# Kernel tuning notes

Measured on AMD Instinct MI355X. Metric: run time of the kernel, lower is better.

Reference implementation:

```python
import jax, jax.numpy as jnp
import numpy as np

N_NODES = 50000
N_EDGES = 800000
D_IN = 256
D_HID = 256
N_CLASSES = 32
N_GRAPHS = 64


def _sage_conv(x, src, dst, W_l, b_l, W_r, num_nodes):
    # PyG SAGEConv (mean aggr, root_weight=True):
    # out = lin_l(mean_{j->i} x_j) + lin_r(x_i)
    msg = x[src]                                                   # [E, d]
    agg = jax.ops.segment_sum(msg, dst, num_segments=num_nodes)   # [N, d]
    cnt = jax.ops.segment_sum(jnp.ones((src.shape[0], 1), x.dtype), dst,
                              num_segments=num_nodes)             # [N, 1]
    agg = agg / jnp.maximum(cnt, 1.0)
    return agg @ W_l + b_l + x @ W_r


def setup_inputs() -> dict:
    key = jax.random.key(0)
    ks = jax.random.split(key, 12)
    x = jax.random.normal(ks[0], (N_NODES, D_IN), dtype=jnp.float32)
    edge_index = jax.random.randint(ks[1], (2, N_EDGES), 0, N_NODES, dtype=jnp.int64)
    batch = jnp.sort(jax.random.randint(ks[2], (N_NODES,), 0, N_GRAPHS, dtype=jnp.int64))
    s1 = 1.0 / np.sqrt(D_IN)
    s2 = 1.0 / np.sqrt(D_HID)
    return {
        "x": x,
        "edge_index": edge_index,
        "batch": batch,
        "W1_l": jax.random.uniform(ks[3], (D_IN, D_HID), jnp.float32, -s1, s1),
        "b1": jax.random.uniform(ks[4], (D_HID,), jnp.float32, -s1, s1),
        "W1_r": jax.random.uniform(ks[5], (D_IN, D_HID), jnp.float32, -s1, s1),
        "W2_l": jax.random.uniform(ks[6], (D_HID, D_HID), jnp.float32, -s2, s2),
        "b2": jax.random.uniform(ks[7], (D_HID,), jnp.float32, -s2, s2),
        "W2_r": jax.random.uniform(ks[8], (D_HID, D_HID), jnp.float32, -s2, s2),
        "Wc": jax.random.uniform(ks[9], (D_HID, N_CLASSES), jnp.float32, -s2, s2),
        "bc": jax.random.uniform(ks[10], (N_CLASSES,), jnp.float32, -s2, s2),
    }


def reference(x, edge_index, batch, W1_l, b1, W1_r, W2_l, b2, W2_r, Wc, bc):
    src, dst = edge_index[0], edge_index[1]
    h = jax.nn.relu(_sage_conv(x, src, dst, W1_l, b1, W1_r, N_NODES))
    h = jax.nn.relu(_sage_conv(h, src, dst, W2_l, b2, W2_r, N_NODES))
    # global mean pool over graphs
    gsum = jax.ops.segment_sum(h, batch, num_segments=N_GRAPHS)        # [G, d]
    gcnt = jax.ops.segment_sum(jnp.ones((h.shape[0], 1), h.dtype), batch,
                               num_segments=N_GRAPHS)                  # [G, 1]
    g = gsum / jnp.maximum(gcnt, 1.0)
    return g @ Wc + bc
```

## Files before the change

kernel.cpp:

```cpp
#include <hip/hip_runtime.h>
#include <stdint.h>

#define NNODES 50000
#define NEDGES 800000
#define DDIM 256
#define NCLS 32
#define NGRAPH 64
#define NSCANB ((NNODES + 255) / 256)
#define HISTB ((NEDGES + 255) / 256)
#define HISTB8 (HISTB * 8)
#define CVTXB ((NNODES * 64 + 255) / 256)
#define CVTWB (2 * 256 * 512 / 256)
#define NPXCD (NNODES / 8)

typedef short bf16x8 __attribute__((ext_vector_type(8)));
typedef float f32x4 __attribute__((ext_vector_type(4)));
typedef unsigned short u16x4 __attribute__((ext_vector_type(4)));
typedef unsigned short u16x8 __attribute__((ext_vector_type(8)));

typedef __attribute__((address_space(1))) const char glb_c;
typedef __attribute__((address_space(3))) char lds_c;


__device__ __forceinline__ unsigned short f2b(float f) {
  uint32_t u = __builtin_bit_cast(uint32_t, f);
  u += 0x7FFFu + ((u >> 16) & 1u);
  return (unsigned short)(u >> 16);
}
__device__ __forceinline__ float b2f(unsigned short u) {
  return __builtin_bit_cast(float, (uint32_t)u << 16);
}
__device__ __forceinline__ float blo(uint32_t u) {
  return __builtin_bit_cast(float, u << 16);
}
__device__ __forceinline__ float bhi(uint32_t u) {
  return __builtin_bit_cast(float, u & 0xFFFF0000u);
}

__device__ __forceinline__ void gload16(const void* g, const void* l) {
  __builtin_amdgcn_global_load_lds((glb_c*)g, (lds_c*)l, 16, 0, 0);
}


__global__ void k_setup(const int* __restrict__ dst, int* __restrict__ cnt,
                        const float* __restrict__ x, unsigned short* __restrict__ xb,
                        const float* __restrict__ W1l, const float* __restrict__ W1r,
                        const float* __restrict__ W2l, const float* __restrict__ W2r,
                        unsigned short* __restrict__ WT1, unsigned short* __restrict__ WT2) {
  int b = blockIdx.x;
  if (b < HISTB8) {
    int xcd = b & 7;
    int e = (b >> 3) * 256 + threadIdx.x;
    if (e < NEDGES) {
      int d = dst[e];
      if ((unsigned)(d - xcd * NPXCD) < (unsigned)NPXCD) atomicAdd(&cnt[d], 1);
    }
  } else if (b < HISTB8 + CVTXB) {
    int i = (b - HISTB8) * 256 + threadIdx.x;
    if (i < NNODES * 64) {
      int seg = i & 7;
      int rr = i >> 3;
      int slab = rr / NNODES;
      int r = rr - slab * NNODES;
      float4 v = *(const float4*)(x + (size_t)r * DDIM + slab * 32 + seg * 4);
      u16x4 o;
      o.x = f2b(v.x); o.y = f2b(v.y); o.z = f2b(v.z); o.w = f2b(v.w);
      *(u16x4*)(xb + (size_t)i * 4) = o;
    }
  } else {
    int idx = (b - HISTB8 - CVTXB) * 256 + threadIdx.x;
    int which = idx >> 17;
    int id2 = idx & 131071;
    int n = id2 >> 9, k = id2 & 511;
    const float* Wl = which ? W2l : W1l;
    const float* Wr = which ? W2r : W1r;
    unsigned short* WT = which ? WT2 : WT1;
    float v = (k < 256) ? Wl[k * 256 + n] : Wr[(k - 256) * 256 + n];
    WT[id2] = f2b(v);
  }
}


__global__ void k_scan1(const int* __restrict__ cnt, int* __restrict__ bsum) {
  int b = blockIdx.x;
  int i = b * 256 + threadIdx.x;
  int lane = threadIdx.x & 63, wid = threadIdx.x >> 6;
  int v = (i < NNODES) ? cnt[i] : 0;
#pragma unroll
  for (int o = 1; o < 64; o <<= 1) v += __shfl_xor(v, o, 64);
  __shared__ int ws[4];
  if (lane == 0) ws[wid] = v;
  __syncthreads();
  if (threadIdx.x == 0) bsum[b] = ws[0] + ws[1] + ws[2] + ws[3];
}

__global__ void k_scan2(const int* __restrict__ bsum, int* __restrict__ boffs) {
  int tid = threadIdx.x, lane = tid & 63, wid = tid >> 6;
  int v = (tid < NSCANB) ? bsum[tid] : 0;
  int s = v;
#pragma unroll
  for (int o = 1; o < 64; o <<= 1) {
    int t = __shfl_up(s, o, 64);
    if (lane >= o) s += t;
  }
  __shared__ int ws[4];
  if (lane == 63) ws[wid] = s;
  __syncthreads();
  int add = 0;
  for (int w = 0; w < wid; ++w) add += ws[w];
  if (tid < NSCANB) boffs[tid] = s + add - v;
}

__global__ void k_scan3(const int* __restrict__ cnt, const int* __restrict__ boffs,
                        int* __restrict__ rowptr, int* __restrict__ cursor,
                        float* __restrict__ gsum, const int* __restrict__ batch,
                        int* __restrict__ gcnt) {
  int b = blockIdx.x;
  if (b < NSCANB) {
    int i = b * 256 + threadIdx.x;
    int lane = threadIdx.x & 63, wid = threadIdx.x >> 6;
    int v = (i < NNODES) ? cnt[i] : 0;
    int s = v;
#pragma unroll
    for (int o = 1; o < 64; o <<= 1) {
      int t = __shfl_up(s, o, 64);
      if (lane >= o) s += t;
    }
    __shared__ int ws[4];
    if (lane == 63) ws[wid] = s;
    __syncthreads();
    int add = boffs[b];
    for (int w = 0; w < wid; ++w) add += ws[w];
    int incl = s + add;
    if (i < NNODES) {
      rowptr[i + 1] = incl;
      cursor[i] = incl - v;
    }
    if (b == 0 && threadIdx.x == 0) rowptr[0] = 0;
  } else if (b == NSCANB) {
    for (int i = threadIdx.x; i < NGRAPH * DDIM; i += 256) gsum[i] = 0.f;
  } else {
    int g = threadIdx.x;
    if (g < NGRAPH) {
      int lo = 0, hi = NNODES;
      while (lo < hi) { int m = (lo + hi) >> 1; if (batch[m] < g) lo = m + 1; else hi = m; }
      int lo2 = lo, hi2 = NNODES;
      while (lo2 < hi2) { int m = (lo2 + hi2) >> 1; if (batch[m] < g + 1) lo2 = m + 1; else hi2 = m; }
      gcnt[g] = lo2 - lo;
    }
  }
}

__global__ void k_fill(const int* __restrict__ src, const int* __restrict__ dst,
                       int* __restrict__ cursor, int* __restrict__ col) {
  int b = blockIdx.x;
  int xcd = b & 7;
  int e = (b >> 3) * 256 + threadIdx.x;
  if (e < NEDGES) {
    int d = dst[e];
    if ((unsigned)(d - xcd * NPXCD) < (unsigned)NPXCD) {
      int p = atomicAdd(&cursor[d], 1);
      col[p] = src[e];
    }
  }
}


__global__ void k_agg(const unsigned short* __restrict__ feat,
                      const int* __restrict__ rowptr, const int* __restrict__ col,
                      unsigned short* __restrict__ out) {
  int g = blockIdx.x & 7;
  int nb = blockIdx.x >> 3;
  int wv = threadIdx.x >> 6, lane = threadIdx.x & 63;
  int ns = lane >> 2;
  int seg = lane & 3;
  int node = nb * 64 + wv * 16 + ns;
  bool valid = node < NNODES;
  int nn = valid ? node : NNODES - 1;
  int s = rowptr[nn], e = rowptr[nn + 1];
  if (!valid) e = s;
  const unsigned short* slabp = feat + (size_t)g * NNODES * 32 + seg * 8;
  float a[8] = {0.f}, b[8] = {0.f};
  int last = e - 1;
  for (int i = s; i < e; i += 8) {
    uint4 vv[8];
#pragma unroll
    for (int j = 0; j < 8; ++j) {
      int idx = i + j;
      int cidx = (idx <= last) ? idx : last;
      int ce = col[cidx];
      uint4 r = *(const uint4*)(slabp + (size_t)ce * 32);
      if (idx > last) { r.x = 0u; r.y = 0u; r.z = 0u; r.w = 0u; }
      vv[j] = r;
    }
#pragma unroll
    for (int j = 0; j < 8; j += 2) {
      a[0] += blo(vv[j].x); a[1] += bhi(vv[j].x);
      a[2] += blo(vv[j].y); a[3] += bhi(vv[j].y);
      a[4] += blo(vv[j].z); a[5] += bhi(vv[j].z);
      a[6] += blo(vv[j].w); a[7] += bhi(vv[j].w);
      b[0] += blo(vv[j + 1].x); b[1] += bhi(vv[j + 1].x);
      b[2] += blo(vv[j + 1].y); b[3] += bhi(vv[j + 1].y);
      b[4] += blo(vv[j + 1].z); b[5] += bhi(vv[j + 1].z);
      b[6] += blo(vv[j + 1].w); b[7] += bhi(vv[j + 1].w);
    }
  }
  if (valid) {
    float inv = (e > s) ? 1.f / (float)(e - s) : 0.f;
    u16x8 o;
#pragma unroll
    for (int j = 0; j < 8; ++j) o[j] = f2b((a[j] + b[j]) * inv);
    unsigned short* op = out + ((size_t)g * NNODES + node) * 32 + seg * 8;
    __builtin_nontemporal_store(o, (u16x8*)op);
  }
}


__global__ void k_gemm(const unsigned short* __restrict__ Aagg,
                       const unsigned short* __restrict__ Aroot,
                       const unsigned short* __restrict__ WT,
                       const float* __restrict__ bias,
                       unsigned short* __restrict__ out) {
  __shared__ unsigned short As[128 * 32];
  __shared__ unsigned short Bs[128 * 32];
  int m0 = blockIdx.x * 128;
  int n0 = blockIdx.y * 128;
  int tid = threadIdx.x, lane = tid & 63, wv = tid >> 6;
  int wm = wv >> 1, wn = wv & 1;

  f32x4 acc[4][4];
#pragma unroll
  for (int m = 0; m < 4; ++m)
#pragma unroll
    for (int n = 0; n < 4; ++n) acc[m][n] = (f32x4)0.f;

  for (int kt = 0; kt < 16; ++kt) {
    int k = kt * 32;
    const unsigned short* Abase = (k < 256) ? Aagg : Aroot;
    int slab = (k & 255) >> 5;
    const unsigned short* Aslab = Abase + (size_t)slab * NNODES * 32;
#pragma unroll
    for (int q = 0; q < 2; ++q) {
      int idx = q * 256 + tid;
      int row = idx >> 2, seg = idx & 3;
      int gr = m0 + row;
      if (gr >= NNODES) gr = NNODES - 1;
      const unsigned short* sp = Aslab + (size_t)gr * 32 + seg * 8;
      gload16(sp, (const char*)As + (q * 256 + wv * 64) * 16);
    }
#pragma unroll
    for (int q = 0; q < 2; ++q) {
      int idx = q * 256 + tid;
      int row = idx >> 2, seg = idx & 3;
      const unsigned short* sp = WT + (size_t)(n0 + row) * 512 + k + seg * 8;
      gload16(sp, (const char*)Bs + (q * 256 + wv * 64) * 16);
    }
    __syncthreads();

    bf16x8 af[4], bfr[4];
    int kb = (lane >> 4) * 8;
    int rA = wm * 64 + (lane & 15);
    int rB = wn * 64 + (lane & 15);
#pragma unroll
    for (int m = 0; m < 4; ++m) af[m] = *(const bf16x8*)&As[(rA + m * 16) * 32 + kb];
#pragma unroll
    for (int n = 0; n < 4; ++n) bfr[n] = *(const bf16x8*)&Bs[(rB + n * 16) * 32 + kb];
#pragma unroll
    for (int m = 0; m < 4; ++m)
#pragma unroll
      for (int n = 0; n < 4; ++n)
        acc[m][n] = __builtin_amdgcn_mfma_f32_16x16x32_bf16(af[m], bfr[n], acc[m][n], 0, 0, 0);
    __syncthreads();
  }

  int rbase = m0 + wm * 64 + (lane >> 4) * 4;
  int cbase = n0 + wn * 64 + (lane & 15);
#pragma unroll
  for (int n = 0; n < 4; ++n) {
    int cc = cbase + n * 16;
    float bv = bias[cc];
    size_t sbase = (size_t)(cc >> 5) * NNODES * 32 + (cc & 31);
#pragma unroll
    for (int m = 0; m < 4; ++m) {
#pragma unroll
      for (int j = 0; j < 4; ++j) {
        int r = rbase + m * 16 + j;
        if (r < NNODES) {
          float v = acc[m][n][j] + bv;
          v = fmaxf(v, 0.f);
          out[sbase + (size_t)r * 32] = f2b(v);
        }
      }
    }
  }
}


#define GSUM_WAVES 1024
__global__ void k_gsum(const unsigned short* __restrict__ h2,
                       const int* __restrict__ batch,
                       float* __restrict__ gsum) {
  int wave = (blockIdx.x * blockDim.x + threadIdx.x) >> 6;
  int lane = threadIdx.x & 63;
  const int per = (NNODES + GSUM_WAVES - 1) / GSUM_WAVES;
  int r0 = wave * per;
  int r1 = r0 + per; if (r1 > NNODES) r1 = NNODES;
  if (r0 >= r1) return;
  int slab = lane >> 3, seg = lane & 7;
  int cb = slab * 32 + seg * 4;
  const unsigned short* sp = h2 + (size_t)slab * NNODES * 32 + seg * 4;
  float a0 = 0.f, a1 = 0.f, a2 = 0.f, a3 = 0.f;
  int cur = batch[r0];
  for (int r = r0; r < r1; ++r) {
    int g = batch[r];
    if (g != cur) {
      float* gp = gsum + cur * DDIM + cb;
      atomicAdd(gp + 0, a0); atomicAdd(gp + 1, a1);
      atomicAdd(gp + 2, a2); atomicAdd(gp + 3, a3);
      a0 = a1 = a2 = a3 = 0.f;
      cur = g;
    }
    u16x4 v = *(const u16x4*)(sp + (size_t)r * 32);
    a0 += b2f(v.x); a1 += b2f(v.y); a2 += b2f(v.z); a3 += b2f(v.w);
  }
  float* gp = gsum + cur * DDIM + cb;
  atomicAdd(gp + 0, a0); atomicAdd(gp + 1, a1);
  atomicAdd(gp + 2, a2); atomicAdd(gp + 3, a3);
}

__global__ void k_cls(const float* __restrict__ gsum, const int* __restrict__ cnt,
                      const float* __restrict__ Wc, const float* __restrict__ bc,
                      float* __restrict__ out) {
  int g = blockIdx.x;
  __shared__ float colmean[DDIM];
  int c = threadIdx.x;
  int n = cnt[g];
  float inv = (n > 0) ? 1.f / (float)n : 0.f;
  colmean[c] = gsum[g * DDIM + c] * inv;
  __syncthreads();
  if (c < NCLS) {
    float o = bc[c];
#pragma unroll 4
    for (int k = 0; k < DDIM; ++k) o += colmean[k] * Wc[k * NCLS + c];
    out[g * NCLS + c] = o;
  }
}


extern "C" void kernel_launch(void* const* d_in, const int* in_sizes, int n_in,
                              void* d_out, int out_size, void* d_ws, size_t ws_size,
                              hipStream_t stream) {
  const float* x    = (const float*)d_in[0];
  const int* eidx   = (const int*)d_in[1];
  const int* batch  = (const int*)d_in[2];
  const float* W1l  = (const float*)d_in[3];
  const float* b1   = (const float*)d_in[4];
  const float* W1r  = (const float*)d_in[5];
  const float* W2l  = (const float*)d_in[6];
  const float* b2   = (const float*)d_in[7];
  const float* W2r  = (const float*)d_in[8];
  const float* Wc   = (const float*)d_in[9];
  const float* bc   = (const float*)d_in[10];
  float* out = (float*)d_out;

  const int* esrc = eidx;
  const int* edst = eidx + NEDGES;

  char* w = (char*)d_ws;
  size_t off = 0;
  auto alloc = [&](size_t bytes) -> char* {
    char* p = w + off;
    off = (off + bytes + 255) & ~(size_t)255;
    return p;
  };
  int* rowptr = (int*)alloc((NNODES + 1) * sizeof(int));
  int* cursor = (int*)alloc(NNODES * sizeof(int));
  int* col    = (int*)alloc(NEDGES * sizeof(int));
  unsigned short* xb   = (unsigned short*)alloc((size_t)NNODES * DDIM * 2);
  unsigned short* h1b  = (unsigned short*)alloc((size_t)NNODES * DDIM * 2);
  unsigned short* aggb = (unsigned short*)alloc((size_t)NNODES * DDIM * 2);
  unsigned short* WT1  = (unsigned short*)alloc(512 * 256 * 2);
  unsigned short* WT2  = (unsigned short*)alloc(512 * 256 * 2);
  float* gsum = (float*)alloc(NGRAPH * DDIM * sizeof(float));
  int* gcnt   = (int*)alloc(NGRAPH * sizeof(int));
  int* bsum   = (int*)alloc(NSCANB * sizeof(int));
  int* boffs  = (int*)alloc(NSCANB * sizeof(int));

  hipMemsetAsync(cursor, 0, NNODES * sizeof(int), stream);
  k_setup<<<HISTB8 + CVTXB + CVTWB, 256, 0, stream>>>(edst, cursor, x, xb,
                                                      W1l, W1r, W2l, W2r, WT1, WT2);
  k_scan1<<<NSCANB, 256, 0, stream>>>(cursor, bsum);
  k_scan2<<<1, 256, 0, stream>>>(bsum, boffs);
  k_scan3<<<NSCANB + 2, 256, 0, stream>>>(cursor, boffs, rowptr, cursor,
                                          gsum, batch, gcnt);
  k_fill<<<HISTB8, 256, 0, stream>>>(esrc, edst, cursor, col);

  dim3 ggrid((NNODES + 127) / 128, 2);
  int agg_grid = ((NNODES + 63) / 64) * 8;

  k_agg<<<agg_grid, 256, 0, stream>>>(xb, rowptr, col, aggb);
  k_gemm<<<ggrid, 256, 0, stream>>>(aggb, xb, WT1, b1, h1b);

  k_agg<<<agg_grid, 256, 0, stream>>>(h1b, rowptr, col, aggb);
  k_gemm<<<ggrid, 256, 0, stream>>>(aggb, h1b, WT2, b2, xb);

  k_gsum<<<GSUM_WAVES / 4, 256, 0, stream>>>(xb, batch, gsum);
  k_cls<<<NGRAPH, 256, 0, stream>>>(gsum, gcnt, Wc, bc, out);
}
```

Measured before the change: 293.5 us.

## Widen GEMM tile to full N with 512 threads; move conversion into fill kernel

The GEMM now uses 512-thread blocks, each covering 128 rows and all 256 output columns. A-tiles are loaded once per row block instead of once per column half, at the cost of a larger B tile in LDS. The x and weight bf16 conversion moves from the histogram kernel into the CSR fill kernel, and the x conversion now reads rows coalesced and scatters into slab layout. The histogram gets its own kernel and count buffer. The aim is to cut redundant A reads and balance the setup kernels.

```diff
diff --git a/kernel.cpp b/kernel.cpp
--- a/kernel.cpp
+++ b/kernel.cpp
@@ -9,7 +9,7 @@
 #define NSCANB ((NNODES + 255) / 256)
 #define HISTB ((NEDGES + 255) / 256)
 #define HISTB8 (HISTB * 8)
-#define CVTXB ((NNODES * 64 + 255) / 256)
+#define CVTXB (NNODES * 64 / 256)
 #define CVTWB (2 * 256 * 512 / 256)
 #define NPXCD (NNODES / 8)
 
@@ -42,44 +42,15 @@
 }
 
 
-__global__ void k_setup(const int* __restrict__ dst, int* __restrict__ cnt,
-                        const float* __restrict__ x, unsigned short* __restrict__ xb,
-                        const float* __restrict__ W1l, const float* __restrict__ W1r,
-                        const float* __restrict__ W2l, const float* __restrict__ W2r,
-                        unsigned short* __restrict__ WT1, unsigned short* __restrict__ WT2) {
+__global__ void k_hist(const int* __restrict__ dst, int* __restrict__ cnt) {
   int b = blockIdx.x;
-  if (b < HISTB8) {
-    int xcd = b & 7;
-    int e = (b >> 3) * 256 + threadIdx.x;
-    if (e < NEDGES) {
-      int d = dst[e];
-      if ((unsigned)(d - xcd * NPXCD) < (unsigned)NPXCD) atomicAdd(&cnt[d], 1);
-    }
-  } else if (b < HISTB8 + CVTXB) {
-    int i = (b - HISTB8) * 256 + threadIdx.x;
-    if (i < NNODES * 64) {
-      int seg = i & 7;
-      int rr = i >> 3;
-      int slab = rr / NNODES;
-      int r = rr - slab * NNODES;
-      float4 v = *(const float4*)(x + (size_t)r * DDIM + slab * 32 + seg * 4);
-      u16x4 o;
-      o.x = f2b(v.x); o.y = f2b(v.y); o.z = f2b(v.z); o.w = f2b(v.w);
-      *(u16x4*)(xb + (size_t)i * 4) = o;
-    }
-  } else {
-    int idx = (b - HISTB8 - CVTXB) * 256 + threadIdx.x;
-    int which = idx >> 17;
-    int id2 = idx & 131071;
-    int n = id2 >> 9, k = id2 & 511;
-    const float* Wl = which ? W2l : W1l;
-    const float* Wr = which ? W2r : W1r;
-    unsigned short* WT = which ? WT2 : WT1;
-    float v = (k < 256) ? Wl[k * 256 + n] : Wr[(k - 256) * 256 + n];
-    WT[id2] = f2b(v);
-  }
-}
-
+  int xcd = b & 7;
+  int e = (b >> 3) * 256 + threadIdx.x;
+  if (e < NEDGES) {
+    int d = dst[e];
+    if ((unsigned)(d - xcd * NPXCD) < (unsigned)NPXCD) atomicAdd(&cnt[d], 1);
+  }
+}
 
 __global__ void k_scan1(const int* __restrict__ cnt, int* __restrict__ bsum) {
   int b = blockIdx.x;
@@ -151,17 +122,42 @@
   }
 }
 
-__global__ void k_fill(const int* __restrict__ src, const int* __restrict__ dst,
-                       int* __restrict__ cursor, int* __restrict__ col) {
+
+__global__ void k_fillcvt(const int* __restrict__ src, const int* __restrict__ dst,
+                          int* __restrict__ cursor, int* __restrict__ col,
+                          const float* __restrict__ x, unsigned short* __restrict__ xb,
+                          const float* __restrict__ W1l, const float* __restrict__ W1r,
+                          const float* __restrict__ W2l, const float* __restrict__ W2r,
+                          unsigned short* __restrict__ WT1, unsigned short* __restrict__ WT2) {
   int b = blockIdx.x;
-  int xcd = b & 7;
-  int e = (b >> 3) * 256 + threadIdx.x;
-  if (e < NEDGES) {
-    int d = dst[e];
-    if ((unsigned)(d - xcd * NPXCD) < (unsigned)NPXCD) {
-      int p = atomicAdd(&cursor[d], 1);
-      col[p] = src[e];
-    }
+  if (b < HISTB8) {
+    int xcd = b & 7;
+    int e = (b >> 3) * 256 + threadIdx.x;
+    if (e < NEDGES) {
+      int d = dst[e];
+      if ((unsigned)(d - xcd * NPXCD) < (unsigned)NPXCD) {
+        int p = atomicAdd(&cursor[d], 1);
+        col[p] = src[e];
+      }
+    }
+  } else if (b < HISTB8 + CVTXB) {
+    int i = (b - HISTB8) * 256 + threadIdx.x;
+    int r = i >> 6, c4 = i & 63;
+    float4 v = *(const float4*)(x + (size_t)r * DDIM + c4 * 4);
+    u16x4 o;
+    o.x = f2b(v.x); o.y = f2b(v.y); o.z = f2b(v.z); o.w = f2b(v.w);
+    int slab = c4 >> 3, seg = c4 & 7;
+    *(u16x4*)(xb + ((size_t)slab * NNODES + r) * 32 + seg * 4) = o;
+  } else {
+    int idx = (b - HISTB8 - CVTXB) * 256 + threadIdx.x;
+    int which = idx >> 17;
+    int id2 = idx & 131071;
+    int n = id2 >> 9, k = id2 & 511;
+    const float* Wl = which ? W2l : W1l;
+    const float* Wr = which ? W2r : W1r;
+    unsigned short* WT = which ? WT2 : WT1;
+    float v = (k < 256) ? Wl[k * 256 + n] : Wr[(k - 256) * 256 + n];
+    WT[id2] = f2b(v);
   }
 }
 
@@ -180,7 +176,7 @@
   int s = rowptr[nn], e = rowptr[nn + 1];
   if (!valid) e = s;
   const unsigned short* slabp = feat + (size_t)g * NNODES * 32 + seg * 8;
-  float a[8] = {0.f}, b[8] = {0.f};
+  float a[8] = {0.f}, bb[8] = {0.f};
   int last = e - 1;
   for (int i = s; i < e; i += 8) {
     uint4 vv[8];
@@ -199,17 +195,17 @@
       a[2] += blo(vv[j].y); a[3] += bhi(vv[j].y);
       a[4] += blo(vv[j].z); a[5] += bhi(vv[j].z);
       a[6] += blo(vv[j].w); a[7] += bhi(vv[j].w);
-      b[0] += blo(vv[j + 1].x); b[1] += bhi(vv[j + 1].x);
-      b[2] += blo(vv[j + 1].y); b[3] += bhi(vv[j + 1].y);
-      b[4] += blo(vv[j + 1].z); b[5] += bhi(vv[j + 1].z);
-      b[6] += blo(vv[j + 1].w); b[7] += bhi(vv[j + 1].w);
+      bb[0] += blo(vv[j + 1].x); bb[1] += bhi(vv[j + 1].x);
+      bb[2] += blo(vv[j + 1].y); bb[3] += bhi(vv[j + 1].y);
+      bb[4] += blo(vv[j + 1].z); bb[5] += bhi(vv[j + 1].z);
+      bb[6] += blo(vv[j + 1].w); bb[7] += bhi(vv[j + 1].w);
     }
   }
   if (valid) {
     float inv = (e > s) ? 1.f / (float)(e - s) : 0.f;
     u16x8 o;
 #pragma unroll
-    for (int j = 0; j < 8; ++j) o[j] = f2b((a[j] + b[j]) * inv);
+    for (int j = 0; j < 8; ++j) o[j] = f2b((a[j] + bb[j]) * inv);
     unsigned short* op = out + ((size_t)g * NNODES + node) * 32 + seg * 8;
     __builtin_nontemporal_store(o, (u16x8*)op);
   }
@@ -222,66 +218,63 @@
                        const float* __restrict__ bias,
                        unsigned short* __restrict__ out) {
   __shared__ unsigned short As[128 * 32];
-  __shared__ unsigned short Bs[128 * 32];
+  __shared__ unsigned short Bs[256 * 32];
   int m0 = blockIdx.x * 128;
-  int n0 = blockIdx.y * 128;
   int tid = threadIdx.x, lane = tid & 63, wv = tid >> 6;
   int wm = wv >> 1, wn = wv & 1;
 
-  f32x4 acc[4][4];
-#pragma unroll
-  for (int m = 0; m < 4; ++m)
-#pragma unroll
-    for (int n = 0; n < 4; ++n) acc[m][n] = (f32x4)0.f;
+  f32x4 acc[2][8];
+#pragma unroll
+  for (int m = 0; m < 2; ++m)
+#pragma unroll
+    for (int n = 0; n < 8; ++n) acc[m][n] = (f32x4)0.f;
 
   for (int kt = 0; kt < 16; ++kt) {
     int k = kt * 32;
-    const unsigned short* Abase = (k < 256) ? Aagg : Aroot;
-    int slab = (k & 255) >> 5;
+    const unsigned short* Abase = (kt < 8) ? Aagg : Aroot;
+    int slab = kt & 7;
     const unsigned short* Aslab = Abase + (size_t)slab * NNODES * 32;
-#pragma unroll
-    for (int q = 0; q < 2; ++q) {
-      int idx = q * 256 + tid;
-      int row = idx >> 2, seg = idx & 3;
+    {
+      int row = tid >> 2, sg = tid & 3;
       int gr = m0 + row;
       if (gr >= NNODES) gr = NNODES - 1;
-      const unsigned short* sp = Aslab + (size_t)gr * 32 + seg * 8;
-      gload16(sp, (const char*)As + (q * 256 + wv * 64) * 16);
-    }
-#pragma unroll
-    for (int q = 0; q < 2; ++q) {
-      int idx = q * 256 + tid;
-      int row = idx >> 2, seg = idx & 3;
-      const unsigned short* sp = WT + (size_t)(n0 + row) * 512 + k + seg * 8;
-      gload16(sp, (const char*)Bs + (q * 256 + wv * 64) * 16);
+      const unsigned short* sp = Aslab + (size_t)gr * 32 + sg * 8;
+      gload16(sp, (const char*)As + (wv * 64) * 16);
+    }
+#pragma unroll
+    for (int p = 0; p < 2; ++p) {
+      int idx = p * 512 + tid;
+      int row = idx >> 2, sg = idx & 3;
+      const unsigned short* sp = WT + (size_t)row * 512 + k + sg * 8;
+      gload16(sp, (const char*)Bs + (p * 512 + wv * 64) * 16);
     }
     __syncthreads();
 
-    bf16x8 af[4], bfr[4];
+    bf16x8 af[2], bfr[8];
     int kb = (lane >> 4) * 8;
-    int rA = wm * 64 + (lane & 15);
-    int rB = wn * 64 + (lane & 15);
-#pragma unroll
-    for (int m = 0; m < 4; ++m) af[m] = *(const bf16x8*)&As[(rA + m * 16) * 32 + kb];
-#pragma unroll
-    for (int n = 0; n < 4; ++n) bfr[n] = *(const bf16x8*)&Bs[(rB + n * 16) * 32 + kb];
-#pragma unroll
-    for (int m = 0; m < 4; ++m)
-#pragma unroll
-      for (int n = 0; n < 4; ++n)
+    int rA = wm * 32 + (lane & 15);
+    int rB = wn * 128 + (lane & 15);
+#pragma unroll
+    for (int m = 0; m < 2; ++m) af[m] = *(const bf16x8*)&As[(rA + m * 16) * 32 + kb];
+#pragma unroll
+    for (int n = 0; n < 8; ++n) bfr[n] = *(const bf16x8*)&Bs[(rB + n * 16) * 32 + kb];
+#pragma unroll
+    for (int m = 0; m < 2; ++m)
+#pragma unroll
+      for (int n = 0; n < 8; ++n)
         acc[m][n] = __builtin_amdgcn_mfma_f32_16x16x32_bf16(af[m], bfr[n], acc[m][n], 0, 0, 0);
     __syncthreads();
   }
 
-  int rbase = m0 + wm * 64 + (lane >> 4) * 4;
-  int cbase = n0 + wn * 64 + (lane & 15);
-#pragma unroll
-  for (int n = 0; n < 4; ++n) {
-    int cc = cbase + n * 16;
+  int rbase = m0 + wm * 32 + (lane >> 4) * 4;
+  int cb = wn * 128 + (lane & 15);
+#pragma unroll
+  for (int n = 0; n < 8; ++n) {
+    int cc = cb + n * 16;
     float bv = bias[cc];
     size_t sbase = (size_t)(cc >> 5) * NNODES * 32 + (cc & 31);
 #pragma unroll
-    for (int m = 0; m < 4; ++m) {
+    for (int m = 0; m < 2; ++m) {
 #pragma unroll
       for (int j = 0; j < 4; ++j) {
         int r = rbase + m * 16 + j;
@@ -374,6 +367,7 @@
     return p;
   };
   int* rowptr = (int*)alloc((NNODES + 1) * sizeof(int));
+  int* cnt    = (int*)alloc(NNODES * sizeof(int));
   int* cursor = (int*)alloc(NNODES * sizeof(int));
   int* col    = (int*)alloc(NEDGES * sizeof(int));
   unsigned short* xb   = (unsigned short*)alloc((size_t)NNODES * DDIM * 2);
@@ -386,23 +380,24 @@
   int* bsum   = (int*)alloc(NSCANB * sizeof(int));
   int* boffs  = (int*)alloc(NSCANB * sizeof(int));
 
-  hipMemsetAsync(cursor, 0, NNODES * sizeof(int), stream);
-  k_setup<<<HISTB8 + CVTXB + CVTWB, 256, 0, stream>>>(edst, cursor, x, xb,
-                                                      W1l, W1r, W2l, W2r, WT1, WT2);
-  k_scan1<<<NSCANB, 256, 0, stream>>>(cursor, bsum);
+  hipMemsetAsync(cnt, 0, NNODES * sizeof(int), stream);
+  k_hist<<<HISTB8, 256, 0, stream>>>(edst, cnt);
+  k_scan1<<<NSCANB, 256, 0, stream>>>(cnt, bsum);
   k_scan2<<<1, 256, 0, stream>>>(bsum, boffs);
-  k_scan3<<<NSCANB + 2, 256, 0, stream>>>(cursor, boffs, rowptr, cursor,
+  k_scan3<<<NSCANB + 2, 256, 0, stream>>>(cnt, boffs, rowptr, cursor,
                                           gsum, batch, gcnt);
-  k_fill<<<HISTB8, 256, 0, stream>>>(esrc, edst, cursor, col);
-
-  dim3 ggrid((NNODES + 127) / 128, 2);
+  k_fillcvt<<<HISTB8 + CVTXB + CVTWB, 256, 0, stream>>>(esrc, edst, cursor, col,
+                                                        x, xb, W1l, W1r, W2l, W2r,
+                                                        WT1, WT2);
+
+  int ggrid = (NNODES + 127) / 128;
   int agg_grid = ((NNODES + 63) / 64) * 8;
 
   k_agg<<<agg_grid, 256, 0, stream>>>(xb, rowptr, col, aggb);
-  k_gemm<<<ggrid, 256, 0, stream>>>(aggb, xb, WT1, b1, h1b);
+  k_gemm<<<ggrid, 512, 0, stream>>>(aggb, xb, WT1, b1, h1b);
 
   k_agg<<<agg_grid, 256, 0, stream>>>(h1b, rowptr, col, aggb);
-  k_gemm<<<ggrid, 256, 0, stream>>>(aggb, h1b, WT2, b2, xb);
+  k_gemm<<<ggrid, 512, 0, stream>>>(aggb, h1b, WT2, b2, xb);
 
   k_gsum<<<GSUM_WAVES / 4, 256, 0, stream>>>(xb, batch, gsum);
   k_cls<<<NGRAPH, 256, 0, stream>>>(gsum, gcnt, Wc, bc, out);
```

Result: no change. 291.7 us (-0.6%).
